# Kernel optimization log

Measured on AMD Instinct MI355X. Metric: run time of the kernel, lower is better.

Reference implementation:

```python
import jax, jax.numpy as jnp
import numpy as np

T = 4096        # tokens
D = 1024        # input_dim
H = 2048        # expert_hidden_dim
O = 1024        # output_dim
E = 8           # num_experts
K = 2           # top_k


def setup_inputs() -> dict:
    key = jax.random.key(0)
    ks = jax.random.split(key, 7)
    s_in = 1.0 / np.sqrt(D)
    s_h = 1.0 / np.sqrt(H)
    return {
        "x": jax.random.normal(ks[0], (T, D), dtype=jnp.float32),
        "Wg": jax.random.uniform(ks[1], (D, E), jnp.float32, -s_in, s_in),
        "bg": jax.random.uniform(ks[2], (E,), jnp.float32, -s_in, s_in),
        "W1": jax.random.uniform(ks[3], (E, D, H), jnp.float32, -s_in, s_in),
        "b1": jax.random.uniform(ks[4], (E, H), jnp.float32, -s_in, s_in),
        "W2": jax.random.uniform(ks[5], (E, H, O), jnp.float32, -s_h, s_h),
        "b2": jax.random.uniform(ks[6], (E, O), jnp.float32, -s_h, s_h),
    }


def reference(x, Wg, bg, W1, b1, W2, b2):
    # Gating: top-k over expert logits, softmax over the k selected logits.
    logits = x @ Wg + bg                                  # [T, E]
    top_vals, top_idx = jax.lax.top_k(logits, K)          # [T, K]
    gates = jax.nn.softmax(top_vals, axis=-1)             # [T, K]

    # Expert MLPs (Linear -> ReLU -> Linear). Each token is processed by the
    # experts it routes to; since an expert's output on x is route-independent,
    # compute all expert outputs once and gather the selected ones (static
    # shapes, jit-friendly equivalent of the masked dispatch loop).
    h = jax.nn.relu(jnp.einsum('td,edh->eth', x, W1) + b1[:, None, :])  # [E,T,H]
    y = jnp.einsum('eth,eho->eto', h, W2) + b2[:, None, :]              # [E,T,O]

    sel = y[top_idx, jnp.arange(T)[:, None]]              # [T, K, O]
    # Weighted combine (scatter_add over batch_idx == per-token sum over K).
    return jnp.sum(sel * gates[..., None], axis=1)        # [T, O]
```

## Files before the change

kernel.cpp:

```cpp
#include <hip/hip_runtime.h>
#include <math.h>


#define T_TOK 4096
#define DIM   1024
#define HID   2048
#define OUTD  1024
#define NE    8

typedef __bf16 bf16_t;
typedef __bf16 bf16x8 __attribute__((ext_vector_type(8)));
typedef float  f32x4  __attribute__((ext_vector_type(4)));

typedef __attribute__((address_space(3))) void       as3_void;
typedef __attribute__((address_space(1))) const void as1_void;
#define GLDS16(src, dst) \
  __builtin_amdgcn_global_load_lds((as1_void*)(src), (as3_void*)(dst), 16, 0, 0)

#define FENCE() asm volatile("" ::: "memory")
#define BARRIER() do { FENCE(); __builtin_amdgcn_s_barrier(); FENCE(); } while (0)
#define LGKM_WAIT() do { \
    asm volatile("s_waitcnt lgkmcnt(0)" ::: "memory"); \
    __builtin_amdgcn_sched_barrier(0); } while (0)
#define VMW_RING() do { \
    if (wid < 4) asm volatile("s_waitcnt vmcnt(4)" ::: "memory"); \
    else         asm volatile("s_waitcnt vmcnt(3)" ::: "memory"); } while (0)
#define VM_WAIT0() asm volatile("s_waitcnt vmcnt(0)" ::: "memory")

__device__ __forceinline__ void gate_body(int bid, const float* __restrict__ x,
                                          const float* __restrict__ Wg,
                                          const float* __restrict__ bg,
                                          int* __restrict__ einfo,
                                          float2* __restrict__ gpair,
                                          bf16_t* __restrict__ xb) {
  int wid  = threadIdx.x >> 6;
  int lane = threadIdx.x & 63;
  int t = bid * 4 + wid;

  const float4* xr = (const float4*)(x + (size_t)t * DIM);
  float4 xv4[4];
  float sf[NE];
#pragma unroll
  for (int e = 0; e < NE; ++e) sf[e] = 0.f;

#pragma unroll
  for (int i = 0; i < 4; ++i) {
    int q = lane + 64 * i;
    float4 xv = xr[q];
    xv4[i] = xv;
    int d = q * 4;
#pragma unroll
    for (int c = 0; c < 4; ++c) {
      float xc = (&xv.x)[c];
      const float4* wr = (const float4*)(Wg + (size_t)(d + c) * NE);
      float4 w0 = wr[0], w1 = wr[1];
      sf[0] += xc * w0.x; sf[1] += xc * w0.y;
      sf[2] += xc * w0.z; sf[3] += xc * w0.w;
      sf[4] += xc * w1.x; sf[5] += xc * w1.y;
      sf[6] += xc * w1.z; sf[7] += xc * w1.w;
    }
  }

  ushort4* xbr = (ushort4*)(xb + (size_t)t * DIM);
#pragma unroll
  for (int i = 0; i < 4; ++i) {
    union { bf16_t b[4]; ushort4 u; } cv;
    cv.b[0] = (bf16_t)xv4[i].x; cv.b[1] = (bf16_t)xv4[i].y;
    cv.b[2] = (bf16_t)xv4[i].z; cv.b[3] = (bf16_t)xv4[i].w;
    xbr[lane + 64 * i] = cv.u;
  }

  double s[NE];
#pragma unroll
  for (int e = 0; e < NE; ++e) s[e] = (double)sf[e];
#pragma unroll
  for (int off = 32; off > 0; off >>= 1) {
#pragma unroll
    for (int e = 0; e < NE; ++e) s[e] += __shfl_xor(s[e], off);
  }

  if (lane == 0) {
    double v0 = -1e300, v1 = -1e300;
    int i0 = 0, i1 = 0;
#pragma unroll
    for (int e = 0; e < NE; ++e) {
      double v = s[e] + (double)bg[e];
      if (v > v0)      { v1 = v0; i1 = i0; v0 = v; i0 = e; }
      else if (v > v1) { v1 = v;  i1 = e; }
    }
    float ex = expf((float)(v1 - v0));
    float inv = 1.0f / (1.0f + ex);
    einfo[t] = i0 | (i1 << 8);
    gpair[t] = make_float2(inv, ex * inv);
  }
}

__device__ __forceinline__ void tr_body(const float* __restrict__ W,
                                        bf16_t* __restrict__ Wt, int R, int C,
                                        int bx, int by, int e, char* lds) {
  size_t ebase = (size_t)e * R * C;
  const int r0 = by * 64, c0 = bx * 128;
  const int tid = threadIdx.x;
#pragma unroll
  for (int half = 0; half < 2; ++half) {
    int b = tid + 256 * half;
    int bc = b & 31, br = b >> 5;
    int r4 = br * 4;
    const float* src = W + ebase + (size_t)(r0 + r4) * C + c0 + bc * 4;
    float4 v0 = *(const float4*)(src);
    float4 v1 = *(const float4*)(src + C);
    float4 v2 = *(const float4*)(src + 2 * (size_t)C);
    float4 v3 = *(const float4*)(src + 3 * (size_t)C);
#pragma unroll
    for (int j = 0; j < 4; ++j) {
      int oc = bc * 4 + j;
      union { bf16_t b4[4]; unsigned long long u; } cv;
      cv.b4[0] = (bf16_t)(&v0.x)[j];
      cv.b4[1] = (bf16_t)(&v1.x)[j];
      cv.b4[2] = (bf16_t)(&v2.x)[j];
      cv.b4[3] = (bf16_t)(&v3.x)[j];
      int cswz = (r4 >> 3) ^ ((oc >> 3) & 7);
      *(unsigned long long*)(lds + oc * 144 + cswz * 16 + (r4 & 7) * 2) = cv.u;
    }
  }
  __syncthreads();
#pragma unroll
  for (int p = 0; p < 4; ++p) {
    int q = tid + 256 * p;
    int oc = q >> 3, seg = q & 7;
    int cswz = seg ^ ((oc >> 3) & 7);
    uint4 val = *(const uint4*)(lds + oc * 144 + cswz * 16);
    *(uint4*)&Wt[ebase + (size_t)(c0 + oc) * R + r0 + seg * 8] = val;
  }
}

#define NB_GATE (T_TOK / 4)
#define NB_TR1  ((DIM / 64) * (HID / 128) * NE)
#define NB_TR2  ((HID / 64) * (OUTD / 128) * NE)
__global__ void k_front(const float* __restrict__ x, const float* __restrict__ Wg,
                        const float* __restrict__ bg, int* __restrict__ einfo,
                        float2* __restrict__ gpair, bf16_t* __restrict__ xb,
                        const float* __restrict__ W1, bf16_t* __restrict__ W1t,
                        const float* __restrict__ W2, bf16_t* __restrict__ W2t) {
  __shared__ __align__(16) char lds[18432];
  int bid = blockIdx.x;
  if (bid < NB_GATE) {
    gate_body(bid, x, Wg, bg, einfo, gpair, xb);
  } else if (bid < NB_GATE + NB_TR1) {
    int i = bid - NB_GATE;
    int nbx = HID / 128, nby = DIM / 64;
    tr_body(W1, W1t, DIM, HID, i % nbx, (i / nbx) % nby, i / (nbx * nby), lds);
  } else {
    int i = bid - NB_GATE - NB_TR1;
    int nbx = OUTD / 128, nby = HID / 64;
    tr_body(W2, W2t, HID, OUTD, i % nbx, (i / nbx) % nby, i / (nbx * nby), lds);
  }
}

__global__ void k_bin(const int* __restrict__ einfo, const float2* __restrict__ gpair,
                      int* __restrict__ cnt, int* __restrict__ offs,
                      int* __restrict__ elist, float* __restrict__ egate,
                      int* __restrict__ tokrec) {
  __shared__ int scnt[NE];
  int w = threadIdx.x >> 6;
  int lane = threadIdx.x & 63;
  unsigned long long below = (lane == 0) ? 0ull : ((~0ull) >> (64 - lane));
  int base = 0;
  for (int c = 0; c < T_TOK / 64; ++c) {
    int t = c * 64 + lane;
    int ei = einfo[t];
    float2 g = gpair[t];
    int e0 = ei & 0xff, e1 = ei >> 8;
    bool m0 = (e0 == w);
    bool m  = m0 || (e1 == w);
    unsigned long long mask = __ballot(m);
    if (m) {
      int pos = base + (int)__popcll(mask & below);
      elist[w * T_TOK + pos] = t;
      egate[w * T_TOK + pos] = m0 ? g.x : g.y;
      tokrec[2 * t + (m0 ? 0 : 1)] = (w << 16) | pos;
    }
    base += (int)__popcll(mask);
  }
  if (lane == 0) scnt[w] = base;
  __syncthreads();
  if (threadIdx.x == 0) {
    int a = 0;
#pragma unroll
    for (int e = 0; e < NE; ++e) {
      cnt[e] = scnt[e];
      offs[e] = a;
      a += scnt[e];
    }
    offs[NE] = a;
  }
}

#define STAGE_A(TT, HH) do { \
    char* _d = smem + (((TT) & 1) * 24576) + ((HH) * 12288); \
    GLDS16(Abase + offA[HH][0] + (TT) * 128, _d + tid * 16); \
    if (tid < 256) GLDS16(Abase + offA[HH][1] + (TT) * 128, _d + (512 + tid) * 16); \
  } while (0)

#define STAGE_B(TT, HH) do { \
    char* _d = smem + 49152 + (((TT) & 1) * 32768) + ((HH) * 16384); \
    GLDS16(Bbase + offB[HH][0] + (TT) * 128, _d + tid * 16); \
    GLDS16(Bbase + offB[HH][1] + (TT) * 128, _d + (512 + tid) * 16); \
  } while (0)

#define MFMA_Q(AF, BF, AH, BH) \
    _Pragma("unroll") for (int i = 0; i < 3; ++i) \
      _Pragma("unroll") for (int j = 0; j < 2; ++j) \
        _Pragma("unroll") for (int kk = 0; kk < 2; ++kk) \
          acc[(AH) * 3 + i][(BH) * 2 + j] = \
            __builtin_amdgcn_mfma_f32_16x16x32_bf16(AF[i][kk], BF[j][kk], \
                acc[(AH) * 3 + i][(BH) * 2 + j], 0, 0, 0)

#define RD_AF(SL) \
    _Pragma("unroll") for (int i = 0; i < 3; ++i) \
      _Pragma("unroll") for (int kk = 0; kk < 2; ++kk) \
        af[i][kk] = *(const bf16x8*)((SL) + rdA[i][kk])

#define KTILE(TT, NTc) do { \
    const char* _a0 = smem + (((TT) & 1) * 24576); \
    const char* _a1 = smem + (((TT) & 1) * 24576) + 12288; \
    const char* _b0 = smem + 49152 + (((TT) & 1) * 32768); \
    const char* _b1 = smem + 49152 + (((TT) & 1) * 32768) + 16384; \
    bf16x8 af[3][2], bf0[2][2], bf1[2][2]; \
    RD_AF(_a0); \
    _Pragma("unroll") for (int j = 0; j < 2; ++j) \
      _Pragma("unroll") for (int kk = 0; kk < 2; ++kk) { \
        bf0[j][kk] = *(const bf16x8*)(_b0 + rdB[j][kk]); \
        bf1[j][kk] = *(const bf16x8*)(_b1 + rdB[j][kk]); \
      } \
    if ((TT) + 1 < (NTc)) { STAGE_A((TT) + 1, 1); STAGE_B((TT) + 1, 1); } \
    BARRIER(); LGKM_WAIT(); \
    __builtin_amdgcn_s_setprio(1); \
    MFMA_Q(af, bf0, 0, 0); MFMA_Q(af, bf1, 0, 1); \
    __builtin_amdgcn_s_setprio(0); BARRIER(); \
    RD_AF(_a1); \
    if ((TT) + 2 < (NTc)) { STAGE_A((TT) + 2, 0); STAGE_B((TT) + 2, 0); \
      VMW_RING(); } \
    else { VM_WAIT0(); } \
    BARRIER(); LGKM_WAIT(); \
    __builtin_amdgcn_s_setprio(1); \
    MFMA_Q(af, bf0, 1, 0); MFMA_Q(af, bf1, 1, 1); \
    __builtin_amdgcn_s_setprio(0); BARRIER(); \
  } while (0)

__launch_bounds__(512, 2)
__global__ void k_gemm1(const bf16_t* __restrict__ xb, const bf16_t* __restrict__ W1t,
                        const float* __restrict__ b1, const int* __restrict__ cnt,
                        const int* __restrict__ offs, const int* __restrict__ elist,
                        bf16_t* __restrict__ hbuf) {
  const int e = blockIdx.z;
  const int count = cnt[e];
  const int rt = blockIdx.y;
  if (rt * 192 >= count) return;
  const int nt = blockIdx.x;

  __shared__ __align__(16) char smem[114688];

  const int tid = threadIdx.x, lane = tid & 63, wid = tid >> 6;
  const int wm = wid >> 2, wn = wid & 3;
  const int fr = lane & 15, lh = lane >> 4;

  unsigned offA[2][2], offB[2][2];
#pragma unroll
  for (int j = 0; j < 2; ++j) {
    int q = j * 512 + tid;
    int r = q >> 3, sfg = (q & 7) ^ (r & 7);
#pragma unroll
    for (int h = 0; h < 2; ++h) {
      int ar = r < 96 ? r : 95;
      int gr = rt * 192 + h * 96 + ar;
      if (gr > count - 1) gr = count - 1;
      int tok = elist[e * T_TOK + gr];
      offA[h][j] = (unsigned)((tok * DIM + sfg * 8) * 2);
      int brow = nt * 256 + h * 128 + r;
      offB[h][j] = (unsigned)(((e * HID + brow) * DIM + sfg * 8) * 2);
    }
  }
  unsigned rdA[3][2], rdB[2][2];
#pragma unroll
  for (int i = 0; i < 3; ++i) {
    int r = wm * 48 + i * 16 + fr;
#pragma unroll
    for (int kk = 0; kk < 2; ++kk)
      rdA[i][kk] = (unsigned)(r * 128 + (((kk * 4 + lh) ^ (r & 7)) * 16));
  }
#pragma unroll
  for (int j = 0; j < 2; ++j) {
    int r = wn * 32 + j * 16 + fr;
#pragma unroll
    for (int kk = 0; kk < 2; ++kk)
      rdB[j][kk] = (unsigned)(r * 128 + (((kk * 4 + lh) ^ (r & 7)) * 16));
  }

  const char* Abase = (const char*)xb;
  const char* Bbase = (const char*)W1t;

  f32x4 acc[6][4];
#pragma unroll
  for (int i = 0; i < 6; ++i)
#pragma unroll
    for (int j = 0; j < 4; ++j) acc[i][j] = (f32x4){0.f, 0.f, 0.f, 0.f};

  const int NT = DIM / 64;
  STAGE_A(0, 0); STAGE_B(0, 0); STAGE_A(0, 1); STAGE_B(0, 1);
  STAGE_A(1, 0); STAGE_B(1, 0);
  VMW_RING();
  BARRIER();

  for (int t = 0; t < NT; ++t) KTILE(t, NT);

  const int hbase = offs[e];
#pragma unroll
  for (int mi = 0; mi < 6; ++mi) {
#pragma unroll
    for (int rr = 0; rr < 4; ++rr) {
      int rowp = rt * 192 + (mi / 3) * 96 + wm * 48 + (mi % 3) * 16 + lh * 4 + rr;
      if (rowp < count) {
        size_t hrow = (size_t)(hbase + rowp) * HID;
#pragma unroll
        for (int nj = 0; nj < 4; ++nj) {
          int col = nt * 256 + (nj >> 1) * 128 + wn * 32 + (nj & 1) * 16 + fr;
          float v = acc[mi][nj][rr] + b1[e * HID + col];
          hbuf[hrow + col] = (bf16_t)(v > 0.f ? v : 0.f);
        }
      }
    }
  }
}

__launch_bounds__(512, 2)
__global__ void k_gemm2(const bf16_t* __restrict__ hbuf, const bf16_t* __restrict__ W2t,
                        const float* __restrict__ b2, const int* __restrict__ cnt,
                        const int* __restrict__ offs, const float* __restrict__ egate,
                        float* __restrict__ y) {
  const int e = blockIdx.z;
  const int count = cnt[e];
  const int rt = blockIdx.y;
  if (rt * 192 >= count) return;
  const int nt = blockIdx.x;

  __shared__ __align__(16) char smem[114688];

  const int tid = threadIdx.x, lane = tid & 63, wid = tid >> 6;
  const int wm = wid >> 2, wn = wid & 3;
  const int fr = lane & 15, lh = lane >> 4;
  const int hbase = offs[e];

  unsigned offA[2][2], offB[2][2];
#pragma unroll
  for (int j = 0; j < 2; ++j) {
    int q = j * 512 + tid;
    int r = q >> 3, sfg = (q & 7) ^ (r & 7);
#pragma unroll
    for (int h = 0; h < 2; ++h) {
      int ar = r < 96 ? r : 95;
      int gr = rt * 192 + h * 96 + ar;
      if (gr > count - 1) gr = count - 1;
      offA[h][j] = (unsigned)(((hbase + gr) * HID + sfg * 8) * 2);
      int brow = nt * 256 + h * 128 + r;
      offB[h][j] = (unsigned)(((e * OUTD + brow) * HID + sfg * 8) * 2);
    }
  }
  unsigned rdA[3][2], rdB[2][2];
#pragma unroll
  for (int i = 0; i < 3; ++i) {
    int r = wm * 48 + i * 16 + fr;
#pragma unroll
    for (int kk = 0; kk < 2; ++kk)
      rdA[i][kk] = (unsigned)(r * 128 + (((kk * 4 + lh) ^ (r & 7)) * 16));
  }
#pragma unroll
  for (int j = 0; j < 2; ++j) {
    int r = wn * 32 + j * 16 + fr;
#pragma unroll
    for (int kk = 0; kk < 2; ++kk)
      rdB[j][kk] = (unsigned)(r * 128 + (((kk * 4 + lh) ^ (r & 7)) * 16));
  }

  const char* Abase = (const char*)hbuf;
  const char* Bbase = (const char*)W2t;

  f32x4 acc[6][4];
#pragma unroll
  for (int i = 0; i < 6; ++i)
#pragma unroll
    for (int j = 0; j < 4; ++j) acc[i][j] = (f32x4){0.f, 0.f, 0.f, 0.f};

  const int NT = HID / 64;
  STAGE_A(0, 0); STAGE_B(0, 0); STAGE_A(0, 1); STAGE_B(0, 1);
  STAGE_A(1, 0); STAGE_B(1, 0);
  VMW_RING();
  BARRIER();

  for (int t = 0; t < NT; ++t) KTILE(t, NT);

#pragma unroll
  for (int mi = 0; mi < 6; ++mi) {
#pragma unroll
    for (int rr = 0; rr < 4; ++rr) {
      int rowp = rt * 192 + (mi / 3) * 96 + wm * 48 + (mi % 3) * 16 + lh * 4 + rr;
      if (rowp < count) {
        float gate = egate[e * T_TOK + rowp];
        size_t yrow = (size_t)(hbase + rowp) * OUTD;
#pragma unroll
        for (int nj = 0; nj < 4; ++nj) {
          int col = nt * 256 + (nj >> 1) * 128 + wn * 32 + (nj & 1) * 16 + fr;
          y[yrow + col] = gate * (acc[mi][nj][rr] + b2[e * OUTD + col]);
        }
      }
    }
  }
}

__global__ void k_combine(const float* __restrict__ y, const int* __restrict__ offs,
                          const int* __restrict__ tokrec, float* __restrict__ out) {
  int t = blockIdx.x;
  int r0 = tokrec[2 * t], r1 = tokrec[2 * t + 1];
  int s0 = offs[r0 >> 16] + (r0 & 0xffff);
  int s1 = offs[r1 >> 16] + (r1 & 0xffff);
  const float4* ya = (const float4*)(y + (size_t)s0 * OUTD);
  const float4* yb = (const float4*)(y + (size_t)s1 * OUTD);
  float4* o = (float4*)(out + (size_t)t * OUTD);
  int i = threadIdx.x;
  float4 a = ya[i], b = yb[i];
  o[i] = make_float4(a.x + b.x, a.y + b.y, a.z + b.z, a.w + b.w);
}

extern "C" void kernel_launch(void* const* d_in, const int* in_sizes, int n_in,
                              void* d_out, int out_size, void* d_ws, size_t ws_size,
                              hipStream_t stream) {
  const float* x  = (const float*)d_in[0];
  const float* Wg = (const float*)d_in[1];
  const float* bg = (const float*)d_in[2];
  const float* W1 = (const float*)d_in[3];
  const float* b1 = (const float*)d_in[4];
  const float* W2 = (const float*)d_in[5];
  const float* b2 = (const float*)d_in[6];
  float* out = (float*)d_out;

  char* ws = (char*)d_ws;
  int*    cnt    = (int*)(ws);
  int*    offs   = (int*)(ws + 1024);
  int*    tokrec = (int*)(ws + 4096);
  int*    einfo  = (int*)(ws + 36864);
  float2* gpair  = (float2*)(ws + 53248);
  int*    elist  = (int*)(ws + 131072);
  float*  egate  = (float*)(ws + 262144);
  bf16_t* W1t    = (bf16_t*)(ws + (1u << 20));
  float*  y      = (float*)(ws + (1u << 20));
  bf16_t* W2t    = (bf16_t*)(ws + (1u << 20) + (32u << 20));
  bf16_t* xb     = (bf16_t*)(ws + (1u << 20) + (64u << 20));
  bf16_t* hbuf   = (bf16_t*)(ws + (1u << 20) + (72u << 20));

  k_front<<<NB_GATE + NB_TR1 + NB_TR2, 256, 0, stream>>>(
      x, Wg, bg, einfo, gpair, xb, W1, W1t, W2, W2t);
  k_bin<<<1, 512, 0, stream>>>(einfo, gpair, cnt, offs, elist, egate, tokrec);

  k_gemm1<<<dim3(HID / 256, 22, NE), 512, 0, stream>>>(
      xb, W1t, b1, cnt, offs, elist, hbuf);
  k_gemm2<<<dim3(OUTD / 256, 22, NE), 512, 0, stream>>>(
      hbuf, W2t, b2, cnt, offs, egate, y);
  k_combine<<<T_TOK, 256, 0, stream>>>(y, offs, tokrec, out);
}
```

Measured before the change: 199.8 us.

## Fuse top-k combine into gemm2 epilogue via atomic adds to output

Removes the intermediate per-slot y buffer and the separate combine kernel; gemm2 now scatters gate-weighted results directly into the token's output row with atomicAdd, after the output is zeroed by a memset. This removes a large fp32 write and re-read plus one launch. In exchange it adds a memset pass and atomic read-modify-write traffic with scattered row addresses.

```diff
diff --git a/kernel.cpp b/kernel.cpp
--- a/kernel.cpp
+++ b/kernel.cpp
@@ -159,8 +159,7 @@
 
 __global__ void k_bin(const int* __restrict__ einfo, const float2* __restrict__ gpair,
                       int* __restrict__ cnt, int* __restrict__ offs,
-                      int* __restrict__ elist, float* __restrict__ egate,
-                      int* __restrict__ tokrec) {
+                      int* __restrict__ elist, float* __restrict__ egate) {
   __shared__ int scnt[NE];
   int w = threadIdx.x >> 6;
   int lane = threadIdx.x & 63;
@@ -178,7 +177,6 @@
       int pos = base + (int)__popcll(mask & below);
       elist[w * T_TOK + pos] = t;
       egate[w * T_TOK + pos] = m0 ? g.x : g.y;
-      tokrec[2 * t + (m0 ? 0 : 1)] = (w << 16) | pos;
     }
     base += (int)__popcll(mask);
   }
@@ -336,8 +334,8 @@
 __launch_bounds__(512, 2)
 __global__ void k_gemm2(const bf16_t* __restrict__ hbuf, const bf16_t* __restrict__ W2t,
                         const float* __restrict__ b2, const int* __restrict__ cnt,
-                        const int* __restrict__ offs, const float* __restrict__ egate,
-                        float* __restrict__ y) {
+                        const int* __restrict__ offs, const int* __restrict__ elist,
+                        const float* __restrict__ egate, float* __restrict__ out) {
   const int e = blockIdx.z;
   const int count = cnt[e];
   const int rt = blockIdx.y;
@@ -405,30 +403,17 @@
     for (int rr = 0; rr < 4; ++rr) {
       int rowp = rt * 192 + (mi / 3) * 96 + wm * 48 + (mi % 3) * 16 + lh * 4 + rr;
       if (rowp < count) {
+        int tokv   = elist[e * T_TOK + rowp];
         float gate = egate[e * T_TOK + rowp];
-        size_t yrow = (size_t)(hbase + rowp) * OUTD;
+        float* orow = out + (size_t)tokv * OUTD;
 #pragma unroll
         for (int nj = 0; nj < 4; ++nj) {
           int col = nt * 256 + (nj >> 1) * 128 + wn * 32 + (nj & 1) * 16 + fr;
-          y[yrow + col] = gate * (acc[mi][nj][rr] + b2[e * OUTD + col]);
+          atomicAdd(&orow[col], gate * (acc[mi][nj][rr] + b2[e * OUTD + col]));
         }
       }
     }
   }
-}
-
-__global__ void k_combine(const float* __restrict__ y, const int* __restrict__ offs,
-                          const int* __restrict__ tokrec, float* __restrict__ out) {
-  int t = blockIdx.x;
-  int r0 = tokrec[2 * t], r1 = tokrec[2 * t + 1];
-  int s0 = offs[r0 >> 16] + (r0 & 0xffff);
-  int s1 = offs[r1 >> 16] + (r1 & 0xffff);
-  const float4* ya = (const float4*)(y + (size_t)s0 * OUTD);
-  const float4* yb = (const float4*)(y + (size_t)s1 * OUTD);
-  float4* o = (float4*)(out + (size_t)t * OUTD);
-  int i = threadIdx.x;
-  float4 a = ya[i], b = yb[i];
-  o[i] = make_float4(a.x + b.x, a.y + b.y, a.z + b.z, a.w + b.w);
 }
 
 extern "C" void kernel_launch(void* const* d_in, const int* in_sizes, int n_in,
@@ -446,24 +431,23 @@
   char* ws = (char*)d_ws;
   int*    cnt    = (int*)(ws);
   int*    offs   = (int*)(ws + 1024);
-  int*    tokrec = (int*)(ws + 4096);
   int*    einfo  = (int*)(ws + 36864);
   float2* gpair  = (float2*)(ws + 53248);
   int*    elist  = (int*)(ws + 131072);
   float*  egate  = (float*)(ws + 262144);
   bf16_t* W1t    = (bf16_t*)(ws + (1u << 20));
-  float*  y      = (float*)(ws + (1u << 20));
   bf16_t* W2t    = (bf16_t*)(ws + (1u << 20) + (32u << 20));
   bf16_t* xb     = (bf16_t*)(ws + (1u << 20) + (64u << 20));
   bf16_t* hbuf   = (bf16_t*)(ws + (1u << 20) + (72u << 20));
 
+  hipMemsetAsync(out, 0, (size_t)out_size * sizeof(float), stream);
+
   k_front<<<NB_GATE + NB_TR1 + NB_TR2, 256, 0, stream>>>(
       x, Wg, bg, einfo, gpair, xb, W1, W1t, W2, W2t);
-  k_bin<<<1, 512, 0, stream>>>(einfo, gpair, cnt, offs, elist, egate, tokrec);
+  k_bin<<<1, 512, 0, stream>>>(einfo, gpair, cnt, offs, elist, egate);
 
   k_gemm1<<<dim3(HID / 256, 22, NE), 512, 0, stream>>>(
       xb, W1t, b1, cnt, offs, elist, hbuf);
   k_gemm2<<<dim3(OUTD / 256, 22, NE), 512, 0, stream>>>(
-      hbuf, W2t, b2, cnt, offs, egate, y);
-  k_combine<<<T_TOK, 256, 0, stream>>>(y, offs, tokrec, out);
-}
+      hbuf, W2t, b2, cnt, offs, elist, egate, out);
+}
```

New measurement: 227.2 us. +13.7%, slower.
